# Performance work log

Hardware: AMD Instinct MI355X
Metric: run time of the kernel (lower is better)

Reference implementation:

```python
import jax, jax.numpy as jnp
import numpy as np


def setup_inputs() -> dict:
    key = jax.random.key(0)
    k1, k2, k3, k4 = jax.random.split(key, 4)
    N_NODES, N_RELS, N_TRIPLES, H = 100000, 100000, 300000, 256
    node_states = jax.random.normal(k1, (N_NODES, H), dtype=jnp.float32)
    rel_states = jax.random.normal(k2, (N_RELS, H), dtype=jnp.float32)
    triples = jax.random.randint(k3, (N_TRIPLES, 3), 0, N_NODES, dtype=jnp.int64)
    # nn.Linear(2H, H): weight (H, 2H) in torch; store transposed (2H, H) for x @ W
    W = jax.random.normal(k4, (2 * H, H), dtype=jnp.float32) * (1.0 / np.sqrt(2 * H))
    b = jnp.zeros((H,), dtype=jnp.float32)
    return {"node_states": node_states, "rel_states": rel_states, "triples": triples, "W": W, "b": b}


def reference(node_states, rel_states, triples, W, b):
    # triples columns: (subj_idx, rel_idx, obj_idx)
    subj_idx, rel_idx, obj_idx = triples[:, 0], triples[:, 1], triples[:, 2]
    rel = rel_states[rel_idx]                              # (T, H)
    msg_s2o = node_states[subj_idx] + rel                  # (T, H)
    msg_o2s = node_states[obj_idx] + rel                   # (T, H)
    agg = jnp.zeros_like(node_states)
    agg = agg.at[obj_idx].add(msg_s2o)
    agg = agg.at[subj_idx].add(msg_o2s)
    h = jnp.concatenate([node_states, agg], axis=-1)       # (N, 2H)
    h = h @ W + b                                          # (N, H)
    h = jax.nn.silu(h)
    return node_states + h
```

## Files before the change

kernel.cpp:

```cpp
#include <hip/hip_runtime.h>

#define H 256
typedef unsigned int  uint;
typedef unsigned short ushort;
typedef float  floatx4 __attribute__((ext_vector_type(4)));
typedef short  shortx8 __attribute__((ext_vector_type(8)));

__device__ __forceinline__ ushort bf16rn(float f) {
    uint u = __float_as_uint(f);
    u += 0x7FFF + ((u >> 16) & 1);
    return (ushort)(u >> 16);
}
__device__ __forceinline__ uint pkbf2(float a, float b) {
    return (uint)bf16rn(a) | ((uint)bf16rn(b) << 16);
}
__device__ __forceinline__ float bf2f(uint lo16) {
    return __uint_as_float(lo16 << 16);
}
__device__ __forceinline__ void atomic_pk_bf16(void* addr, uint v) {
    asm volatile("global_atomic_pk_add_bf16 %0, %1, off" :: "v"(addr), "v"(v) : "memory");
}
__device__ __forceinline__ void glds16(const void* g, void* l) {
    __builtin_amdgcn_global_load_lds(
        (__attribute__((address_space(1))) void*)(unsigned long long)(g),
        (__attribute__((address_space(3))) void*)(l), 16, 0, 0);
}

__global__ __launch_bounds__(256) void wt_kernel(const float* __restrict__ W,
                                                 ushort* __restrict__ Wt) {
    int k = blockIdx.x;
    int n = threadIdx.x;
    Wt[(size_t)n * 512 + k] = bf16rn(W[(size_t)k * H + n]);
}

__global__ __launch_bounds__(256) void prep_kernel(const float* __restrict__ ns,
                                                   char* __restrict__ outbase, int M)
{
    int row = blockIdx.x * 2 + (threadIdx.x >> 7);
    if (row >= M) return;
    int t = threadIdx.x & 127;
    float2 v = ((const float2*)ns)[(size_t)row * 128 + t];
    uint* rp = (uint*)(outbase + (size_t)row * 1024);
    rp[t]       = 0u;
    rp[128 + t] = pkbf2(v.x, v.y);
}

__global__ __launch_bounds__(256) void scatter_kernel(
    const float* __restrict__ rs, const int* __restrict__ trip,
    char* __restrict__ outbase, int n_trip)
{
    int t = blockIdx.x * 2 + (threadIdx.x >> 7);
    if (t >= n_trip) return;
    int p = threadIdx.x & 127;
    int s = trip[3 * t + 0];
    int r = trip[3 * t + 1];
    int o = trip[3 * t + 2];
    uint bs = *(const uint*)(outbase + (size_t)s * 1024 + 512 + p * 4);
    uint bo = *(const uint*)(outbase + (size_t)o * 1024 + 512 + p * 4);
    float2 vr = ((const float2*)rs)[(size_t)r * 128 + p];
    uint m_s2o = pkbf2(bf2f(bs & 0xffffu) + vr.x, bf2f(bs >> 16) + vr.y);
    uint m_o2s = pkbf2(bf2f(bo & 0xffffu) + vr.x, bf2f(bo >> 16) + vr.y);
    atomic_pk_bf16(outbase + (size_t)o * 1024 + p * 4, m_s2o);
    atomic_pk_bf16(outbase + (size_t)s * 1024 + p * 4, m_o2s);
}

__global__ __launch_bounds__(256) void gemm_kernel(
    const float* __restrict__ ns, const char* __restrict__ arows,
    const ushort* __restrict__ Wt, const float* __restrict__ bias,
    float* __restrict__ out, int M)
{
    __shared__ __align__(16) ushort As[64 * 32];
    __shared__ __align__(16) ushort Bs[256 * 32];

    const int tid  = threadIdx.x;
    const int wave = tid >> 6;
    const int lane = tid & 63;
    const int fm = lane & 15, fq = lane >> 4;
    const int rowBase = blockIdx.x * 64;

    floatx4 acc[4][4] = {};

    const int am = tid >> 2, akq = tid & 3;
    int arow = rowBase + am; if (arow >= M) arow = M - 1;
    const char* asrc = arows + (size_t)arow * 1024 + akq * 16;
    const char* wtp  = (const char*)Wt;

#pragma unroll
    for (int kt = 0; kt < 16; ++kt) {
        __syncthreads();
        glds16(asrc + ((512 + kt * 64) & 1023), &As[tid * 8]);
#pragma unroll
        for (int j = 0; j < 4; ++j)
            glds16(wtp + (size_t)(j * 64 + am) * 1024 + kt * 64 + akq * 16,
                   &Bs[j * 2048 + tid * 8]);
        __syncthreads();

        shortx8 aF[4], bF[4];
#pragma unroll
        for (int mi = 0; mi < 4; ++mi)
            aF[mi] = *(const shortx8*)&As[(mi * 16 + fm) * 32 + fq * 8];
#pragma unroll
        for (int ni = 0; ni < 4; ++ni)
            bF[ni] = *(const shortx8*)&Bs[(wave * 64 + ni * 16 + fm) * 32 + fq * 8];
#pragma unroll
        for (int mi = 0; mi < 4; ++mi)
#pragma unroll
            for (int ni = 0; ni < 4; ++ni)
                acc[mi][ni] = __builtin_amdgcn_mfma_f32_16x16x32_bf16(
                    aF[mi], bF[ni], acc[mi][ni], 0, 0, 0);
    }

#pragma unroll
    for (int mi = 0; mi < 4; ++mi) {
#pragma unroll
        for (int ni = 0; ni < 4; ++ni) {
            int col = wave * 64 + ni * 16 + fm;
            float bc = bias[col];
#pragma unroll
            for (int r = 0; r < 4; ++r) {
                int row = rowBase + mi * 16 + fq * 4 + r;
                if (row < M) {
                    float x = acc[mi][ni][r] + bc;
                    float sg = 1.f / (1.f + __expf(-x));
                    out[(size_t)row * H + col] = ns[(size_t)row * H + col] + x * sg;
                }
            }
        }
    }
}

extern "C" void kernel_launch(void* const* d_in, const int* in_sizes, int n_in,
                              void* d_out, int out_size, void* d_ws, size_t ws_size,
                              hipStream_t stream)
{
    const float* ns   = (const float*)d_in[0];
    const float* rs   = (const float*)d_in[1];
    const int*   tp   = (const int*)d_in[2];
    const float* Wm   = (const float*)d_in[3];
    const float* bias = (const float*)d_in[4];
    const int M      = in_sizes[0] / H;
    const int n_trip = in_sizes[2] / 3;
    float*  out = (float*)d_out;
    ushort* Wt  = (ushort*)d_ws;

    prep_kernel<<<dim3((M + 1) / 2), dim3(256), 0, stream>>>(ns, (char*)out, M);
    wt_kernel<<<dim3(512), dim3(256), 0, stream>>>(Wm, Wt);
    scatter_kernel<<<dim3((n_trip + 1) / 2), dim3(256), 0, stream>>>(
        rs, tp, (char*)out, n_trip);
    gemm_kernel<<<dim3((M + 63) / 64), dim3(256), 0, stream>>>(
        ns, (const char*)out, Wt, bias, out, M);
}
```

Measured before the change: 600.9 us.

## Double-buffer GEMM tiles with 128-row blocks and pre-tiled weight layout

The GEMM now uses 512-thread blocks, each covering 128 rows with a 2x4 wave grid, so every staged weight tile is reused across twice as many rows. The A and B tiles are double-buffered in LDS, and the next k-tile is prefetched while the current one is in the matrix cores, which removes one barrier per iteration. The weight transpose kernel goes through a shared-memory tile and writes Wt in a [kt][n][32] layout, so each B stage is one contiguous block. LDS use per block doubles, and the scatter kernel, which probably dominates the total time, is untouched.

```diff
diff --git a/kernel.cpp b/kernel.cpp
--- a/kernel.cpp
+++ b/kernel.cpp
@@ -28,9 +28,22 @@
 
 __global__ __launch_bounds__(256) void wt_kernel(const float* __restrict__ W,
                                                  ushort* __restrict__ Wt) {
-    int k = blockIdx.x;
-    int n = threadIdx.x;
-    Wt[(size_t)n * 512 + k] = bf16rn(W[(size_t)k * H + n]);
+    __shared__ ushort tile[64][65];
+    int k0 = (blockIdx.x >> 2) * 64;
+    int n0 = (blockIdx.x & 3) * 64;
+    int tx = threadIdx.x & 63, ty = threadIdx.x >> 6;
+#pragma unroll
+    for (int i = 0; i < 16; ++i) {
+        int k = ty + i * 4;
+        tile[k][tx] = bf16rn(W[(size_t)(k0 + k) * H + n0 + tx]);
+    }
+    __syncthreads();
+#pragma unroll
+    for (int i = 0; i < 16; ++i) {
+        int n = ty + i * 4;
+        int k = k0 + tx;
+        Wt[(size_t)((k >> 5) * 256 + n0 + n) * 32 + (k & 31)] = tile[tx][n];
+    }
 }
 
 __global__ __launch_bounds__(256) void prep_kernel(const float* __restrict__ ns,
@@ -64,19 +77,20 @@
     atomic_pk_bf16(outbase + (size_t)s * 1024 + p * 4, m_o2s);
 }
 
-__global__ __launch_bounds__(256) void gemm_kernel(
+__global__ __launch_bounds__(512) void gemm_kernel(
     const float* __restrict__ ns, const char* __restrict__ arows,
     const ushort* __restrict__ Wt, const float* __restrict__ bias,
     float* __restrict__ out, int M)
 {
-    __shared__ __align__(16) ushort As[64 * 32];
-    __shared__ __align__(16) ushort Bs[256 * 32];
+    __shared__ __align__(16) ushort As[2][128 * 32];
+    __shared__ __align__(16) ushort Bs[2][256 * 32];
 
     const int tid  = threadIdx.x;
     const int wave = tid >> 6;
     const int lane = tid & 63;
     const int fm = lane & 15, fq = lane >> 4;
-    const int rowBase = blockIdx.x * 64;
+    const int wm = wave >> 2, wn = wave & 3;
+    const int rowBase = blockIdx.x * 128;
 
     floatx4 acc[4][4] = {};
 
@@ -85,40 +99,49 @@
     const char* asrc = arows + (size_t)arow * 1024 + akq * 16;
     const char* wtp  = (const char*)Wt;
 
+#define STAGE(kt, buf)                                                        \
+    do {                                                                      \
+        glds16(asrc + ((512 + (kt) * 64) & 1023), &As[(buf)][tid * 8]);       \
+        glds16(wtp + (size_t)(kt) * 16384 + tid * 16, &Bs[(buf)][tid * 8]);   \
+        glds16(wtp + (size_t)(kt) * 16384 + 8192 + tid * 16,                  \
+               &Bs[(buf)][4096 + tid * 8]);                                   \
+    } while (0)
+
+    STAGE(0, 0);
+    __syncthreads();
+
 #pragma unroll
     for (int kt = 0; kt < 16; ++kt) {
-        __syncthreads();
-        glds16(asrc + ((512 + kt * 64) & 1023), &As[tid * 8]);
-#pragma unroll
-        for (int j = 0; j < 4; ++j)
-            glds16(wtp + (size_t)(j * 64 + am) * 1024 + kt * 64 + akq * 16,
-                   &Bs[j * 2048 + tid * 8]);
-        __syncthreads();
+        const int cur = kt & 1;
+        if (kt < 15) STAGE(kt + 1, cur ^ 1);
 
         shortx8 aF[4], bF[4];
 #pragma unroll
         for (int mi = 0; mi < 4; ++mi)
-            aF[mi] = *(const shortx8*)&As[(mi * 16 + fm) * 32 + fq * 8];
+            aF[mi] = *(const shortx8*)&As[cur][(wm * 64 + mi * 16 + fm) * 32 + fq * 8];
 #pragma unroll
         for (int ni = 0; ni < 4; ++ni)
-            bF[ni] = *(const shortx8*)&Bs[(wave * 64 + ni * 16 + fm) * 32 + fq * 8];
+            bF[ni] = *(const shortx8*)&Bs[cur][(wn * 64 + ni * 16 + fm) * 32 + fq * 8];
 #pragma unroll
         for (int mi = 0; mi < 4; ++mi)
 #pragma unroll
             for (int ni = 0; ni < 4; ++ni)
                 acc[mi][ni] = __builtin_amdgcn_mfma_f32_16x16x32_bf16(
                     aF[mi], bF[ni], acc[mi][ni], 0, 0, 0);
+
+        __syncthreads();
     }
+#undef STAGE
 
 #pragma unroll
     for (int mi = 0; mi < 4; ++mi) {
 #pragma unroll
         for (int ni = 0; ni < 4; ++ni) {
-            int col = wave * 64 + ni * 16 + fm;
+            int col = wn * 64 + ni * 16 + fm;
             float bc = bias[col];
 #pragma unroll
             for (int r = 0; r < 4; ++r) {
-                int row = rowBase + mi * 16 + fq * 4 + r;
+                int row = rowBase + wm * 64 + mi * 16 + fq * 4 + r;
                 if (row < M) {
                     float x = acc[mi][ni][r] + bc;
                     float sg = 1.f / (1.f + __expf(-x));
@@ -144,9 +167,9 @@
     ushort* Wt  = (ushort*)d_ws;
 
     prep_kernel<<<dim3((M + 1) / 2), dim3(256), 0, stream>>>(ns, (char*)out, M);
-    wt_kernel<<<dim3(512), dim3(256), 0, stream>>>(Wm, Wt);
+    wt_kernel<<<dim3(32), dim3(256), 0, stream>>>(Wm, Wt);
     scatter_kernel<<<dim3((n_trip + 1) / 2), dim3(256), 0, stream>>>(
         rs, tp, (char*)out, n_trip);
-    gemm_kernel<<<dim3((M + 63) / 64), dim3(256), 0, stream>>>(
+    gemm_kernel<<<dim3((M + 127) / 128), dim3(512), 0, stream>>>(
         ns, (const char*)out, Wt, bias, out, M);
 }
```

After: 583.2 us. 1.03x faster.
